# Kernel tuning notes

Measured on AMD Instinct MI355X. Metric: run time of the kernel, lower is better.

Reference implementation:

```python
import jax, jax.numpy as jnp
import numpy as np

N_HEADS = 16
HEAD_DIM = 64
ROPE_THETA = 10000.0


def rotate_half(x):
    x1, x2 = jnp.split(x, 2, axis=-1)
    return jnp.concatenate([-x2, x1], axis=-1)


def setup_inputs() -> dict:
    key = jax.random.key(0)
    k0, k1, k2 = jax.random.split(key, 3)
    B, L, C = 2, 2048, 1024
    x = jax.random.normal(k0, (B, L, C), dtype=jnp.float32)
    # causal additive bias, as used by VAR-style blockwise masks (here full causal)
    causal = jnp.tril(jnp.ones((L, L), dtype=bool))
    attn_bias = jnp.where(causal, 0.0, -1e9).astype(jnp.float32)[None, None]
    position_ids = jnp.broadcast_to(jnp.arange(L, dtype=jnp.int32), (B, L))
    qkv_w = 0.02 * jax.random.normal(k1, (3 * C, C), dtype=jnp.float32)
    q_bias = jnp.zeros((C,), jnp.float32)
    v_bias = jnp.zeros((C,), jnp.float32)
    proj_w = 0.02 * jax.random.normal(k2, (C, C), dtype=jnp.float32)
    proj_b = jnp.zeros((C,), jnp.float32)
    return {"x": x, "attn_bias": attn_bias, "position_ids": position_ids,
            "qkv_w": qkv_w, "q_bias": q_bias, "v_bias": v_bias,
            "proj_w": proj_w, "proj_b": proj_b}


def reference(x, attn_bias, position_ids, qkv_w, q_bias, v_bias, proj_w, proj_b):
    B, L, C = x.shape
    H, D = N_HEADS, HEAD_DIM
    # fused QKV projection with concatenated (q_bias, 0, v_bias)
    bias = jnp.concatenate([q_bias, jnp.zeros_like(q_bias), v_bias])
    qkv = (jnp.einsum('blc,oc->blo', x, qkv_w) + bias).reshape(B, L, 3, H, D)
    q = jnp.transpose(qkv[:, :, 0], (0, 2, 1, 3))  # [B,H,L,D]
    k = jnp.transpose(qkv[:, :, 1], (0, 2, 1, 3))
    v = jnp.transpose(qkv[:, :, 2], (0, 2, 1, 3))
    # Llama rotary embedding: cos/sin [B,L,D] -> unsqueeze dim=1
    inv_freq = 1.0 / (ROPE_THETA ** (jnp.arange(0, D, 2, dtype=jnp.float32) / D))
    freqs = position_ids.astype(jnp.float32)[:, :, None] * inv_freq  # [B,L,D/2]
    emb = jnp.concatenate([freqs, freqs], axis=-1)
    cos = jnp.cos(emb)[:, None]  # [B,1,L,D]
    sin = jnp.sin(emb)[:, None]
    q = q * cos + rotate_half(q) * sin
    k = k * cos + rotate_half(k) * sin
    # slow_attn: (q*scale) @ k^T + bias -> softmax -> @ v
    scale = 0.25 / np.sqrt(D).astype(np.float32)
    attn = jnp.einsum('bhqd,bhkd->bhqk', q * scale, k) + attn_bias
    attn = jax.nn.softmax(attn, axis=-1)
    out = jnp.einsum('bhqk,bhkd->bhqd', attn, v)
    out = out.transpose(0, 2, 1, 3).reshape(B, L, C)
    return jnp.einsum('blc,oc->blo', out, proj_w) + proj_b
```

## Files before the change

kernel.cpp:

```cpp
#include <hip/hip_runtime.h>

typedef unsigned short u16;
typedef unsigned int u32;
typedef __attribute__((ext_vector_type(8))) short short8;
typedef __attribute__((ext_vector_type(4))) float f32x4;
typedef __attribute__((ext_vector_type(2))) unsigned int u32x2;
typedef __attribute__((ext_vector_type(4))) unsigned short u16x4;
typedef __attribute__((ext_vector_type(8))) unsigned short u16x8;

#define AS1 __attribute__((address_space(1)))
#define AS3 __attribute__((address_space(3)))

__device__ __forceinline__ u16 f2bf(float f) {
  u32 u = __builtin_bit_cast(u32, f);
  u32 r = u + 0x7FFFu + ((u >> 16) & 1u);
  return (u16)(r >> 16);
}
__device__ __forceinline__ float bf2f(u16 h) {
  u32 u = ((u32)h) << 16;
  return __builtin_bit_cast(float, u);
}
__device__ __forceinline__ void gload_lds16(const void* g, void* l) {
  __builtin_amdgcn_global_load_lds((AS1 void*)g, (AS3 void*)l, 16, 0, 0);
}
__device__ __forceinline__ float fexp2(float x) {
  float r;
  asm("v_exp_f32 %0, %1" : "=v"(r) : "v"(x));
  return r;
}

#define QSCALE 0.04508422002778011f

__device__ __forceinline__ void cvt_body(const float* __restrict__ src, u16* __restrict__ dst,
                                         int i) {
  float4 v = ((const float4*)src)[i];
  u16x4 o;
  o[0] = f2bf(v.x); o[1] = f2bf(v.y); o[2] = f2bf(v.z); o[3] = f2bf(v.w);
  ((u16x4*)dst)[i] = o;
}

__global__ __launch_bounds__(256)
void pre_kernel(const float* __restrict__ x, const float* __restrict__ w1,
                const float* __restrict__ w2, const int* __restrict__ pos,
                u16* __restrict__ x_bf, u16* __restrict__ w1_bf, u16* __restrict__ w2_bf,
                float* __restrict__ tab) {
  int bid = blockIdx.x;
  int t = threadIdx.x;
  if (bid < 4096) {
    cvt_body(x, x_bf, bid * 256 + t);
  } else if (bid < 7168) {
    cvt_body(w1, w1_bf, (bid - 4096) * 256 + t);
  } else if (bid < 8192) {
    cvt_body(w2, w2_bf, (bid - 7168) * 256 + t);
  } else {
    int idx = (bid - 8192) * 256 + t;
    int i = idx & 31;
    int bl = idx >> 5;
    float p = (float)pos[bl];
    float inv_freq = 1.0f / powf(10000.0f, (2.0f * (float)i) / 64.0f);
    float ang = p * inv_freq;
    tab[(size_t)bl * 64 + i] = cosf(ang);
    tab[(size_t)bl * 64 + 32 + i] = sinf(ang);
  }
}

template <bool OUT_BF16>
__global__ __launch_bounds__(256)
void gemm_bt_kernel(const u16* __restrict__ A, const u16* __restrict__ Bw,
                    void* __restrict__ Cout, const float* __restrict__ bias,
                    int M, int N, int K, int NXT) {
  __shared__ alignas(16) u16 As[128 * 64];
  __shared__ alignas(16) u16 Bs[128 * 64];
  const int tid = threadIdx.x;
  const int lane = tid & 63, wave = tid >> 6;
  const int wr = wave >> 1, wc = wave & 1;
  const int nblk = gridDim.x;
  const int lin = (blockIdx.x & 7) * (nblk >> 3) + (blockIdx.x >> 3);
  const int m0 = (lin / NXT) * 128, n0 = (lin % NXT) * 128;
  const int r = lane & 15, g = lane >> 4;

  f32x4 acc[4][4] = {};

  const int nk = K >> 6;
  for (int kt = 0; kt < nk; ++kt) {
    const int k0 = kt << 6;
#pragma unroll
    for (int c = 0; c < 4; ++c) {
      int i = c * 256 + tid;
      int row = i >> 3, slot = i & 7;
      int ss = slot ^ (row & 7);
      const u16* gA = A + (size_t)(m0 + row) * K + k0 + ss * 8;
      const u16* gB = Bw + (size_t)(n0 + row) * K + k0 + ss * 8;
      void* lA = (char*)As + c * 4096 + wave * 1024;
      void* lB = (char*)Bs + c * 4096 + wave * 1024;
      gload_lds16(gA, lA);
      gload_lds16(gB, lB);
    }
    __syncthreads();
#pragma unroll
    for (int kk = 0; kk < 2; ++kk) {
      short8 af[4], bf[4];
#pragma unroll
      for (int m = 0; m < 4; ++m) {
        int row = wr * 64 + m * 16 + r;
        int byte = row * 128 + (((kk * 4 + g) ^ (row & 7)) << 4);
        af[m] = *(const short8*)((const char*)As + byte);
      }
#pragma unroll
      for (int n = 0; n < 4; ++n) {
        int row = wc * 64 + n * 16 + r;
        int byte = row * 128 + (((kk * 4 + g) ^ (row & 7)) << 4);
        bf[n] = *(const short8*)((const char*)Bs + byte);
      }
#pragma unroll
      for (int m = 0; m < 4; ++m)
#pragma unroll
        for (int n = 0; n < 4; ++n)
          acc[m][n] = __builtin_amdgcn_mfma_f32_16x16x32_bf16(af[m], bf[n], acc[m][n], 0, 0, 0);
    }
    __syncthreads();
  }

  if constexpr (OUT_BF16) {
    u16* C = (u16*)Cout;
#pragma unroll
    for (int m = 0; m < 4; ++m) {
      int rg = m0 + wr * 64 + m * 16 + g * 4;
#pragma unroll
      for (int n = 0; n < 4; ++n) {
        int cg = n0 + wc * 64 + n * 16 + r;
#pragma unroll
        for (int j = 0; j < 4; ++j)
          C[(size_t)(rg + j) * N + cg] = f2bf(acc[m][n][j]);
      }
    }
  } else {
    float* C = (float*)Cout;
#pragma unroll
    for (int m = 0; m < 4; ++m) {
      int rg = m0 + wr * 64 + m * 16 + g * 4;
#pragma unroll
      for (int n = 0; n < 4; ++n) {
        int cg = n0 + wc * 64 + n * 16 + r;
        float bv = bias[cg];
#pragma unroll
        for (int j = 0; j < 4; ++j)
          C[(size_t)(rg + j) * N + cg] = acc[m][n][j] + bv;
      }
    }
  }
}

__global__ __launch_bounds__(256)
void gemm_bt64_kernel(const u16* __restrict__ A, const u16* __restrict__ Bw,
                      float* __restrict__ Cout, const float* __restrict__ bias,
                      int M, int N, int K, int NXT) {
  __shared__ alignas(16) u16 As[128 * 64];
  __shared__ alignas(16) u16 Bs[64 * 64];
  const int tid = threadIdx.x;
  const int lane = tid & 63, wave = tid >> 6;
  const int wr = wave >> 1, wc = wave & 1;
  const int nblk = gridDim.x;
  const int lin = (blockIdx.x & 7) * (nblk >> 3) + (blockIdx.x >> 3);
  const int m0 = (lin / NXT) * 128, n0 = (lin % NXT) * 64;
  const int r = lane & 15, g = lane >> 4;

  f32x4 acc[4][2] = {};

  const int nk = K >> 6;
  for (int kt = 0; kt < nk; ++kt) {
    const int k0 = kt << 6;
#pragma unroll
    for (int c = 0; c < 4; ++c) {
      int i = c * 256 + tid;
      int row = i >> 3, slot = i & 7;
      int ss = slot ^ (row & 7);
      const u16* gA = A + (size_t)(m0 + row) * K + k0 + ss * 8;
      void* lA = (char*)As + c * 4096 + wave * 1024;
      gload_lds16(gA, lA);
    }
#pragma unroll
    for (int c = 0; c < 2; ++c) {
      int i = c * 256 + tid;
      int row = i >> 3, slot = i & 7;
      int ss = slot ^ (row & 7);
      const u16* gB = Bw + (size_t)(n0 + row) * K + k0 + ss * 8;
      void* lB = (char*)Bs + c * 4096 + wave * 1024;
      gload_lds16(gB, lB);
    }
    __syncthreads();
#pragma unroll
    for (int kk = 0; kk < 2; ++kk) {
      short8 af[4], bf[2];
#pragma unroll
      for (int m = 0; m < 4; ++m) {
        int row = wr * 64 + m * 16 + r;
        int byte = row * 128 + (((kk * 4 + g) ^ (row & 7)) << 4);
        af[m] = *(const short8*)((const char*)As + byte);
      }
#pragma unroll
      for (int n = 0; n < 2; ++n) {
        int row = wc * 32 + n * 16 + r;
        int byte = row * 128 + (((kk * 4 + g) ^ (row & 7)) << 4);
        bf[n] = *(const short8*)((const char*)Bs + byte);
      }
#pragma unroll
      for (int m = 0; m < 4; ++m)
#pragma unroll
        for (int n = 0; n < 2; ++n)
          acc[m][n] = __builtin_amdgcn_mfma_f32_16x16x32_bf16(af[m], bf[n], acc[m][n], 0, 0, 0);
    }
    __syncthreads();
  }

#pragma unroll
  for (int m = 0; m < 4; ++m) {
    int rg = m0 + wr * 64 + m * 16 + g * 4;
#pragma unroll
    for (int n = 0; n < 2; ++n) {
      int cg = n0 + wc * 32 + n * 16 + r;
      float bv = bias[cg];
#pragma unroll
      for (int j = 0; j < 4; ++j)
        Cout[(size_t)(rg + j) * N + cg] = acc[m][n][j] + bv;
    }
  }
}

__global__ __launch_bounds__(256)
void mid_kernel(const u16* __restrict__ qkv, const float* __restrict__ tab,
                const float* __restrict__ q_bias, const float* __restrict__ v_bias,
                u16* __restrict__ Qo, u16* __restrict__ Ko, u16* __restrict__ vt) {
  __shared__ alignas(16) u16 tile[64][72];
  int bid = blockIdx.x;
  int t = threadIdx.x;
  if (bid < 4096) {
    int bl = bid;
    int b = bl >> 11, l = bl & 2047;
    const float* tr = tab + (size_t)bl * 64;
    const u16* base = qkv + (size_t)bl * 3072;
#pragma unroll
    for (int pp = 0; pp < 2; ++pp) {
      int p = t + pp * 256;
      int h = p >> 5, d = p & 31;
      float c = tr[d], s = tr[32 + d];
      size_t o = ((size_t)(b * 16 + h) * 2048 + l) * 64 + d;
      float x1 = bf2f(base[h * 64 + d]) + q_bias[h * 64 + d];
      float x2 = bf2f(base[h * 64 + d + 32]) + q_bias[h * 64 + d + 32];
      Qo[o]      = f2bf((x1 * c - x2 * s) * QSCALE);
      Qo[o + 32] = f2bf((x2 * c + x1 * s) * QSCALE);
      x1 = bf2f(base[1024 + h * 64 + d]);
      x2 = bf2f(base[1024 + h * 64 + d + 32]);
      Ko[o]      = f2bf(x1 * c - x2 * s);
      Ko[o + 32] = f2bf(x2 * c + x1 * s);
    }
  } else {
    int bid2 = bid - 4096;
    int bh = bid2 >> 5;
    int b = bh >> 4, h = bh & 15;
    int l0 = (bid2 & 31) * 64;
    int rr = t >> 2;
    int c0 = (t & 3) * 16;
    const u16* src = qkv + ((size_t)(b * 2048 + l0 + rr)) * 3072 + 2048 + h * 64 + c0;
    u16x8 a = *(const u16x8*)src;
    u16x8 bb = *(const u16x8*)(src + 8);
#pragma unroll
    for (int i = 0; i < 8; ++i) {
      a[i]  = f2bf(bf2f(a[i])  + v_bias[h * 64 + c0 + i]);
      bb[i] = f2bf(bf2f(bb[i]) + v_bias[h * 64 + c0 + 8 + i]);
    }
    *(u16x8*)&tile[rr][c0] = a;
    *(u16x8*)&tile[rr][c0 + 8] = bb;
    __syncthreads();
    int d = t >> 2;
    int lc = (t & 3) * 16;
    u16x8 o1, o2;
#pragma unroll
    for (int i = 0; i < 8; ++i) {
      o1[i] = tile[lc + i][d];
      o2[i] = tile[lc + 8 + i][d];
    }
    u16* dst = vt + ((size_t)bh * 64 + d) * 2048 + l0 + lc;
    *(u16x8*)dst = o1;
    *(u16x8*)(dst + 8) = o2;
  }
}

__global__ __launch_bounds__(512)
void attn_kernel(const u16* __restrict__ Q, const u16* __restrict__ Kmat,
                 const u16* __restrict__ Vt, u16* __restrict__ O) {
  __shared__ alignas(16) u16 Ks[3][64 * 64];
  __shared__ alignas(16) u16 Vs[3][64 * 64];
  __shared__ alignas(16) u16 Pbuf[8][1024];
  const int tid = threadIdx.x;
  const int lane = tid & 63;
  const int wave = tid >> 6;
  const int id = blockIdx.x;
  const int xcd = id & 7, rank = id >> 3;
  const int bh = xcd + 8 * (rank & 3);
  const int xq = 15 - (rank >> 2);
  const int ntA = 2 * xq + 2;
  const int b = bh >> 4, h = bh & 15;
  const int r = lane & 15, g = lane >> 4;

  const u16* Kb = Kmat + (size_t)bh * 2048 * 64;
  const u16* Vb = Vt + (size_t)bh * 64 * 2048;

  const int srow = wave * 8 + (lane >> 3);
  const int sslot = (lane & 7) ^ (srow & 7);

#define STAGE(tt, bb) do { \
    gload_lds16(Kb + ((size_t)((tt) * 64 + srow)) * 64 + sslot * 8, \
                (char*)Ks[bb] + wave * 1024); \
    gload_lds16(Vb + (size_t)srow * 2048 + (tt) * 64 + sslot * 8, \
                (char*)Vs[bb] + wave * 1024); \
  } while (0)

  u16* Pw = Pbuf[wave];
  const int qrow0 = xq * 128 + wave * 16;
  const int nt = (qrow0 + 79) >> 6;
  const u16* Qb = Q + ((size_t)bh * 2048 + qrow0) * 64;

  short8 qf[2];
#pragma unroll
  for (int kk = 0; kk < 2; ++kk)
    qf[kk] = *(const short8*)(Qb + r * 64 + kk * 32 + g * 8);

  short8 ones;
#pragma unroll
  for (int i = 0; i < 8; ++i) ones[i] = (short)0x3F80;

  f32x4 o_acc[4] = {};
  f32x4 l_acc = {};

  STAGE(0, 0);
  STAGE(1, 1);
  asm volatile("s_waitcnt vmcnt(2)" ::: "memory");
  __builtin_amdgcn_s_barrier();

  for (int t = 0; t < ntA; ++t) {
    if (t + 2 < ntA) STAGE(t + 2, (t + 2) % 3);

    if (t < nt) {
      const char* Kc = (const char*)Ks[t % 3];
      const char* Vc = (const char*)Vs[t % 3];
      const int kv0 = t * 64;

      f32x4 s[4] = {};
      __builtin_amdgcn_s_setprio(1);
#pragma unroll
      for (int ct = 0; ct < 4; ++ct) {
#pragma unroll
        for (int kk = 0; kk < 2; ++kk) {
          int row = ct * 16 + r;
          int byte = row * 128 + (((kk * 4 + g) ^ (row & 7)) << 4);
          short8 kf = *(const short8*)(Kc + byte);
          s[ct] = __builtin_amdgcn_mfma_f32_16x16x32_bf16(kf, qf[kk], s[ct], 0, 0, 0);
        }
      }
      __builtin_amdgcn_s_setprio(0);

      if (kv0 + 63 > qrow0) {
        int qrow = qrow0 + r;
#pragma unroll
        for (int ct = 0; ct < 4; ++ct)
#pragma unroll
          for (int j = 0; j < 4; ++j) {
            int kv = kv0 + ct * 16 + 4 * g + j;
            if (kv > qrow) s[ct][j] = -1e30f;
          }
      }

      u32x2 pk[4];
#pragma unroll
      for (int ct = 0; ct < 4; ++ct) {
        float p0 = fexp2(s[ct][0]);
        float p1 = fexp2(s[ct][1]);
        float p2 = fexp2(s[ct][2]);
        float p3 = fexp2(s[ct][3]);
        u32 lo, hi;
        asm("v_cvt_pk_bf16_f32 %0, %1, %2" : "=v"(lo) : "v"(p0), "v"(p1));
        asm("v_cvt_pk_bf16_f32 %0, %1, %2" : "=v"(hi) : "v"(p2), "v"(p3));
        pk[ct][0] = lo;
        pk[ct][1] = hi;
      }

#pragma unroll
      for (int ct = 0; ct < 4; ++ct) {
        int byte = r * 128 + ((32 * ct + 8 * g) ^ ((r & 7) << 4));
        *(u32x2*)((char*)Pw + byte) = pk[ct];
      }

      __builtin_amdgcn_s_setprio(1);
#pragma unroll
      for (int kk = 0; kk < 2; ++kk) {
        int byte = r * 128 + (((kk * 4 + g) ^ (r & 7)) << 4);
        short8 pf = *(const short8*)((const char*)Pw + byte);
        l_acc = __builtin_amdgcn_mfma_f32_16x16x32_bf16(pf, ones, l_acc, 0, 0, 0);
#pragma unroll
        for (int n = 0; n < 4; ++n) {
          int row = n * 16 + r;
          int vbyte = row * 128 + (((kk * 4 + g) ^ (row & 7)) << 4);
          short8 vf = *(const short8*)(Vc + vbyte);
          o_acc[n] = __builtin_amdgcn_mfma_f32_16x16x32_bf16(pf, vf, o_acc[n], 0, 0, 0);
        }
      }
      __builtin_amdgcn_s_setprio(0);
    }

    if (t + 1 < ntA) {
      if (t + 2 < ntA) {
        asm volatile("s_waitcnt vmcnt(2)" ::: "memory");
      } else {
        asm volatile("s_waitcnt vmcnt(0)" ::: "memory");
      }
      __builtin_amdgcn_s_barrier();
    }
  }
#undef STAGE

  float ij[4];
#pragma unroll
  for (int j = 0; j < 4; ++j) ij[j] = 1.0f / l_acc[j];
#pragma unroll
  for (int n = 0; n < 4; ++n)
#pragma unroll
    for (int j = 0; j < 4; ++j) {
      size_t idx = ((size_t)b * 2048 + qrow0 + 4 * g + j) * 1024 + h * 64 + n * 16 + r;
      O[idx] = f2bf(o_acc[n][j] * ij[j]);
    }
}

extern "C" void kernel_launch(void* const* d_in, const int* in_sizes, int n_in,
                              void* d_out, int out_size, void* d_ws, size_t ws_size,
                              hipStream_t stream) {
  const float* x      = (const float*)d_in[0];
  const int*   pos    = (const int*)d_in[2];
  const float* qkv_w  = (const float*)d_in[3];
  const float* q_bias = (const float*)d_in[4];
  const float* v_bias = (const float*)d_in[5];
  const float* proj_w = (const float*)d_in[6];
  const float* proj_b = (const float*)d_in[7];
  float* out = (float*)d_out;

  char* ws = (char*)d_ws;
  u16* x_bf    = (u16*)(ws + 0);
  u16* w1_bf   = (u16*)(ws + 8388608);
  u16* w2_bf   = (u16*)(ws + 14680064);
  u16* qkv_bf  = (u16*)(ws + 16777216);
  u16* q_bf    = (u16*)(ws + 41943040);
  u16* k_bf    = (u16*)(ws + 50331648);
  u16* vt_bf   = (u16*)(ws + 58720256);
  u16* attn_bf = (u16*)(ws + 67108864);
  float* tab   = (float*)(ws + 75497472);

  pre_kernel<<<8704, 256, 0, stream>>>(x, qkv_w, proj_w, pos, x_bf, w1_bf, w2_bf, tab);
  gemm_bt_kernel<true><<<768, 256, 0, stream>>>(x_bf, w1_bf, qkv_bf, nullptr,
                                                4096, 3072, 1024, 24);
  mid_kernel<<<5120, 256, 0, stream>>>(qkv_bf, tab, q_bias, v_bias, q_bf, k_bf, vt_bf);
  attn_kernel<<<512, 512, 0, stream>>>(q_bf, k_bf, vt_bf, attn_bf);
  gemm_bt64_kernel<<<512, 256, 0, stream>>>(attn_bf, w2_bf, out, proj_b,
                                            4096, 1024, 1024, 16);
}
```

Measured before the change: 115.0 us.

## Split attention KV range across two wave groups and vectorize RoPE kernel

The attention kernel now gives each block 64 query rows instead of 128 and splits the KV tiles between two groups of four waves. Each group processes alternate tiles from a four-buffer LDS ring, and the partial O and row-sum accumulators are merged through LDS at the end. The grid doubles to 1024 blocks, which improves load balance and occupancy under the causal triangle, at the cost of a final reduction and full vmcnt(0) waits per step. The RoPE part of mid_kernel is also rewritten to use vectorized 4-element loads and stores per thread, with Q and K split across thread halves.

```diff
diff --git a/kernel.cpp b/kernel.cpp
--- a/kernel.cpp
+++ b/kernel.cpp
@@ -239,21 +239,37 @@
     int b = bl >> 11, l = bl & 2047;
     const float* tr = tab + (size_t)bl * 64;
     const u16* base = qkv + (size_t)bl * 3072;
-#pragma unroll
-    for (int pp = 0; pp < 2; ++pp) {
-      int p = t + pp * 256;
-      int h = p >> 5, d = p & 31;
-      float c = tr[d], s = tr[32 + d];
-      size_t o = ((size_t)(b * 16 + h) * 2048 + l) * 64 + d;
-      float x1 = bf2f(base[h * 64 + d]) + q_bias[h * 64 + d];
-      float x2 = bf2f(base[h * 64 + d + 32]) + q_bias[h * 64 + d + 32];
-      Qo[o]      = f2bf((x1 * c - x2 * s) * QSCALE);
-      Qo[o + 32] = f2bf((x2 * c + x1 * s) * QSCALE);
-      x1 = bf2f(base[1024 + h * 64 + d]);
-      x2 = bf2f(base[1024 + h * 64 + d + 32]);
-      Ko[o]      = f2bf(x1 * c - x2 * s);
-      Ko[o + 32] = f2bf(x2 * c + x1 * s);
-    }
+    const int tensor = t >> 7;
+    const int rem = t & 127;
+    const int h = rem >> 3;
+    const int d0 = (rem & 7) * 4;
+    const u16* src = base + tensor * 1024 + h * 64 + d0;
+    u16x4 a1 = *(const u16x4*)src;
+    u16x4 a2 = *(const u16x4*)(src + 32);
+    float4 vc = *(const float4*)(tr + d0);
+    float4 vs = *(const float4*)(tr + 32 + d0);
+    float4 b1 = {0.f, 0.f, 0.f, 0.f}, b2 = b1;
+    if (tensor == 0) {
+      b1 = *(const float4*)(q_bias + h * 64 + d0);
+      b2 = *(const float4*)(q_bias + h * 64 + d0 + 32);
+    }
+    const float sc = (tensor == 0) ? QSCALE : 1.0f;
+    float c4[4] = {vc.x, vc.y, vc.z, vc.w};
+    float s4[4] = {vs.x, vs.y, vs.z, vs.w};
+    float bb1[4] = {b1.x, b1.y, b1.z, b1.w};
+    float bb2[4] = {b2.x, b2.y, b2.z, b2.w};
+    u16x4 o1, o2;
+#pragma unroll
+    for (int i = 0; i < 4; ++i) {
+      float x1 = bf2f(a1[i]) + bb1[i];
+      float x2 = bf2f(a2[i]) + bb2[i];
+      o1[i] = f2bf((x1 * c4[i] - x2 * s4[i]) * sc);
+      o2[i] = f2bf((x2 * c4[i] + x1 * s4[i]) * sc);
+    }
+    u16* Out = (tensor == 0) ? Qo : Ko;
+    size_t o = ((size_t)(b * 16 + h) * 2048 + l) * 64 + d0;
+    *(u16x4*)(Out + o) = o1;
+    *(u16x4*)(Out + o + 32) = o2;
   } else {
     int bid2 = bid - 4096;
     int bh = bid2 >> 5;
@@ -289,17 +305,20 @@
 __global__ __launch_bounds__(512)
 void attn_kernel(const u16* __restrict__ Q, const u16* __restrict__ Kmat,
                  const u16* __restrict__ Vt, u16* __restrict__ O) {
-  __shared__ alignas(16) u16 Ks[3][64 * 64];
-  __shared__ alignas(16) u16 Vs[3][64 * 64];
+  __shared__ alignas(16) u16 Ks[4][64 * 64];
+  __shared__ alignas(16) u16 Vs[4][64 * 64];
   __shared__ alignas(16) u16 Pbuf[8][1024];
   const int tid = threadIdx.x;
   const int lane = tid & 63;
   const int wave = tid >> 6;
+  const int grp = wave >> 2;
+  const int w4 = wave & 3;
   const int id = blockIdx.x;
   const int xcd = id & 7, rank = id >> 3;
   const int bh = xcd + 8 * (rank & 3);
-  const int xq = 15 - (rank >> 2);
-  const int ntA = 2 * xq + 2;
+  const int xq = 31 - (rank >> 2);
+  const int nt = xq + 1;
+  const int nss = (nt + 1) >> 1;
   const int b = bh >> 4, h = bh & 15;
   const int r = lane & 15, g = lane >> 4;
 
@@ -317,8 +336,7 @@
   } while (0)
 
   u16* Pw = Pbuf[wave];
-  const int qrow0 = xq * 128 + wave * 16;
-  const int nt = (qrow0 + 79) >> 6;
+  const int qrow0 = xq * 64 + w4 * 16;
   const u16* Qb = Q + ((size_t)bh * 2048 + qrow0) * 64;
 
   short8 qf[2];
@@ -335,15 +353,21 @@
 
   STAGE(0, 0);
   STAGE(1, 1);
-  asm volatile("s_waitcnt vmcnt(2)" ::: "memory");
+  asm volatile("s_waitcnt vmcnt(0)" ::: "memory");
   __builtin_amdgcn_s_barrier();
 
-  for (int t = 0; t < ntA; ++t) {
-    if (t + 2 < ntA) STAGE(t + 2, (t + 2) % 3);
-
+  for (int ss = 0; ss < nss; ++ss) {
+    const int t0 = 2 * ss;
+    const int cb = 2 * (ss & 1);
+    const int sb = 2 * ((ss + 1) & 1);
+
+    if (t0 + 2 < nt) STAGE(t0 + 2, sb);
+    if (t0 + 3 < nt) STAGE(t0 + 3, sb + 1);
+
+    const int t = t0 + grp;
     if (t < nt) {
-      const char* Kc = (const char*)Ks[t % 3];
-      const char* Vc = (const char*)Vs[t % 3];
+      const char* Kc = (const char*)Ks[cb + grp];
+      const char* Vc = (const char*)Vs[cb + grp];
       const int kv0 = t * 64;
 
       f32x4 s[4] = {};
@@ -378,11 +402,8 @@
         float p1 = fexp2(s[ct][1]);
         float p2 = fexp2(s[ct][2]);
         float p3 = fexp2(s[ct][3]);
-        u32 lo, hi;
-        asm("v_cvt_pk_bf16_f32 %0, %1, %2" : "=v"(lo) : "v"(p0), "v"(p1));
-        asm("v_cvt_pk_bf16_f32 %0, %1, %2" : "=v"(hi) : "v"(p2), "v"(p3));
-        pk[ct][0] = lo;
-        pk[ct][1] = hi;
+        asm("v_cvt_pk_bf16_f32 %0, %1, %2" : "=v"(pk[ct][0]) : "v"(p0), "v"(p1));
+        asm("v_cvt_pk_bf16_f32 %0, %1, %2" : "=v"(pk[ct][1]) : "v"(p2), "v"(p3));
       }
 
 #pragma unroll
@@ -408,27 +429,44 @@
       __builtin_amdgcn_s_setprio(0);
     }
 
-    if (t + 1 < ntA) {
-      if (t + 2 < ntA) {
-        asm volatile("s_waitcnt vmcnt(2)" ::: "memory");
-      } else {
-        asm volatile("s_waitcnt vmcnt(0)" ::: "memory");
-      }
+    if (ss + 1 < nss) {
+      asm volatile("s_waitcnt vmcnt(0)" ::: "memory");
       __builtin_amdgcn_s_barrier();
     }
   }
 #undef STAGE
 
-  float ij[4];
-#pragma unroll
-  for (int j = 0; j < 4; ++j) ij[j] = 1.0f / l_acc[j];
-#pragma unroll
-  for (int n = 0; n < 4; ++n)
-#pragma unroll
-    for (int j = 0; j < 4; ++j) {
-      size_t idx = ((size_t)b * 2048 + qrow0 + 4 * g + j) * 1024 + h * 64 + n * 16 + r;
-      O[idx] = f2bf(o_acc[n][j] * ij[j]);
-    }
+  __builtin_amdgcn_s_barrier();
+  float* mbase = (float*)(char*)Ks[0];
+  float* slot = mbase + (size_t)(w4 * 64 + lane) * 21;
+  if (grp == 1) {
+#pragma unroll
+    for (int n = 0; n < 4; ++n)
+#pragma unroll
+      for (int j = 0; j < 4; ++j) slot[n * 4 + j] = o_acc[n][j];
+#pragma unroll
+    for (int j = 0; j < 4; ++j) slot[16 + j] = l_acc[j];
+  }
+  __builtin_amdgcn_s_barrier();
+  if (grp == 0) {
+#pragma unroll
+    for (int n = 0; n < 4; ++n)
+#pragma unroll
+      for (int j = 0; j < 4; ++j) o_acc[n][j] += slot[n * 4 + j];
+#pragma unroll
+    for (int j = 0; j < 4; ++j) l_acc[j] += slot[16 + j];
+
+    float ij[4];
+#pragma unroll
+    for (int j = 0; j < 4; ++j) ij[j] = 1.0f / l_acc[j];
+#pragma unroll
+    for (int n = 0; n < 4; ++n)
+#pragma unroll
+      for (int j = 0; j < 4; ++j) {
+        size_t idx = ((size_t)b * 2048 + qrow0 + 4 * g + j) * 1024 + h * 64 + n * 16 + r;
+        O[idx] = f2bf(o_acc[n][j] * ij[j]);
+      }
+  }
 }
 
 extern "C" void kernel_launch(void* const* d_in, const int* in_sizes, int n_in,
@@ -458,7 +496,7 @@
   gemm_bt_kernel<true><<<768, 256, 0, stream>>>(x_bf, w1_bf, qkv_bf, nullptr,
                                                 4096, 3072, 1024, 24);
   mid_kernel<<<5120, 256, 0, stream>>>(qkv_bf, tab, q_bias, v_bias, q_bf, k_bf, vt_bf);
-  attn_kernel<<<512, 512, 0, stream>>>(q_bf, k_bf, vt_bf, attn_bf);
+  attn_kernel<<<1024, 512, 0, stream>>>(q_bf, k_bf, vt_bf, attn_bf);
   gemm_bt64_kernel<<<512, 256, 0, stream>>>(attn_bf, w2_bf, out, proj_b,
                                             4096, 1024, 1024, 16);
 }
```

Measured after the change: 105.8 us (median of 3 runs). 8.0% less time.
